# Optimization experiments

Measured on AMD Instinct MI355X. Metric: run time of the kernel, lower is better.

The kernel has to match this reference:

```python
import jax, jax.numpy as jnp
import numpy as np
import math

B, S, D, H = 4, 2048, 1024, 16
DK = D // H


def _rope_tables(seq_len, dim, dtype=jnp.float32):
    inv_freq = 1.0 / (10000.0 ** (jnp.arange(0, dim, 2, dtype=jnp.float32) / dim))
    t = jnp.arange(seq_len, dtype=jnp.float32)
    freqs = jnp.einsum('i,j->ij', t, inv_freq)          # [S, dim/2]
    emb = jnp.concatenate([freqs, freqs], axis=-1)       # [S, dim]
    return jnp.cos(emb).astype(dtype)[None, None], jnp.sin(emb).astype(dtype)[None, None]


def _apply_rope(x, cos, sin):
    # faithful to source: rotated = cat([-x[...,1::2], x[...,::2]], -1)
    x_rot = jnp.concatenate([-x[..., 1::2], x[..., ::2]], axis=-1)
    return x * cos + x_rot * sin


def setup_inputs() -> dict:
    key = jax.random.key(0)
    ks = jax.random.split(key, 12)
    scale = 1.0 / math.sqrt(D)
    inp = {
        'query': jax.random.normal(ks[0], (B, S, D), jnp.float32),
        'key':   jax.random.normal(ks[1], (B, S, D), jnp.float32),
        'value': jax.random.normal(ks[2], (B, S, D), jnp.float32),
        'mask':  jnp.tril(jnp.ones((S, S), jnp.int32))[None, None],  # causal [1,1,S,S]
        'w_q': jax.random.normal(ks[3], (D, D), jnp.float32) * scale,
        'b_q': jnp.zeros((D,), jnp.float32),
        'w_k': jax.random.normal(ks[4], (D, D), jnp.float32) * scale,
        'b_k': jnp.zeros((D,), jnp.float32),
        'w_v': jax.random.normal(ks[5], (D, D), jnp.float32) * scale,
        'b_v': jnp.zeros((D,), jnp.float32),
        'w_o': jax.random.normal(ks[6], (D, D), jnp.float32) * scale,
        'b_o': jnp.zeros((D,), jnp.float32),
    }
    return inp


def reference(query, key, value, mask, w_q, b_q, w_k, b_k, w_v, b_v, w_o, b_o):
    b, s, _ = query.shape
    # projections (torch Linear: x @ W.T + b), split heads -> [B,H,S,Dk]
    def proj(x, w, bias):
        return (x @ w.T + bias).reshape(b, -1, H, DK).transpose(0, 2, 1, 3)
    Q = proj(query, w_q, b_q)
    K = proj(key, w_k, b_k)
    V = proj(value, w_v, b_v)
    cos, sin = _rope_tables(s, DK, Q.dtype)
    Q = _apply_rope(Q, cos, sin)
    K = _apply_rope(K, cos, sin)
    scores = jnp.einsum('bhqd,bhkd->bhqk', Q, K) / math.sqrt(DK)
    scores = jnp.where(mask == 0, jnp.asarray(-1e9, scores.dtype), scores)
    attn = jax.nn.softmax(scores, axis=-1)
    ctx = jnp.einsum('bhqk,bhkd->bhqd', attn, V)
    ctx = ctx.transpose(0, 2, 1, 3).reshape(b, -1, D)
    return ctx @ w_o.T + b_o
```

## Files before the change

### kernel.cpp

```cpp
#include <hip/hip_runtime.h>
#include <hip/hip_bf16.h>
#include <math.h>

#define B_  4
#define S_  2048
#define D_  1024
#define H_  16
#define DK_ 64
#define M_  (B_ * S_)

typedef short short8 __attribute__((ext_vector_type(8)));
typedef float floatx4 __attribute__((ext_vector_type(4)));

__device__ inline unsigned short f2bf(float x) {
    unsigned u = __float_as_uint(x);
    u = (u + 0x7fff + ((u >> 16) & 1)) >> 16;
    return (unsigned short)u;
}
__device__ inline float bf2f(unsigned short h) {
    return __uint_as_float(((unsigned)h) << 16);
}

__device__ inline unsigned cvt_pk_bf16(float lo, float hi) {
    unsigned r;
    asm("v_cvt_pk_bf16_f32 %0, %1, %2" : "=v"(r) : "v"(lo), "v"(hi));
    return r;
}

template <int K>
__device__ inline float dpp_ror(float x) {
    return __uint_as_float((unsigned)__builtin_amdgcn_update_dpp(
        0, (int)__float_as_uint(x), 0x120 | K, 0xF, 0xF, true));
}
__device__ inline float rowmax16(float x) {
    x = fmaxf(x, dpp_ror<8>(x));
    x = fmaxf(x, dpp_ror<4>(x));
    x = fmaxf(x, dpp_ror<2>(x));
    x = fmaxf(x, dpp_ror<1>(x));
    return x;
}
__device__ inline float rowsum16(float x) {
    x += dpp_ror<8>(x);
    x += dpp_ror<4>(x);
    x += dpp_ror<2>(x);
    x += dpp_ror<1>(x);
    return x;
}

#define GLOAD_LDS16(g, l)                                          \
    __builtin_amdgcn_global_load_lds(                              \
        (const __attribute__((address_space(1))) void*)(g),        \
        (__attribute__((address_space(3))) void*)(l), 16, 0, 0)

__global__ __launch_bounds__(256) void cvt_inputs_kernel(
    const float* __restrict__ q, const float* __restrict__ k,
    const float* __restrict__ v, unsigned short* __restrict__ Ah)
{
    const int z = blockIdx.z;
    const float* src = (z == 0) ? q : (z == 1) ? k : v;
    unsigned short* dst = Ah + (size_t)z * M_ * D_;
    const size_t i = ((size_t)blockIdx.x * 256 + threadIdx.x) * 4;
    float4 f = *(const float4*)(src + i);
    ushort4 o;
    o.x = f2bf(f.x); o.y = f2bf(f.y); o.z = f2bf(f.z); o.w = f2bf(f.w);
    *(ushort4*)(dst + i) = o;
}

__global__ __launch_bounds__(256) void cvt_weights_kernel(
    const float* __restrict__ wq, const float* __restrict__ wk,
    const float* __restrict__ wv, const float* __restrict__ wo,
    unsigned short* __restrict__ Wh, unsigned short* __restrict__ Woh)
{
    const int z = blockIdx.z;
    const float* src = (z == 0) ? wq : (z == 1) ? wk : (z == 2) ? wv : wo;
    unsigned short* dst = (z < 3) ? (Wh + (size_t)z * D_ * D_) : Woh;
    const size_t i = ((size_t)blockIdx.x * 256 + threadIdx.x) * 4;
    float4 f = *(const float4*)(src + i);
    ushort4 o;
    o.x = f2bf(f.x); o.y = f2bf(f.y); o.z = f2bf(f.z); o.w = f2bf(f.w);
    *(ushort4*)(dst + i) = o;
}

template <int MODE>
__global__ __launch_bounds__(256) void gemm_bf16_kernel(
    const unsigned short* __restrict__ Ah, const unsigned short* __restrict__ Wh,
    const float* __restrict__ bq, const float* __restrict__ bk,
    const float* __restrict__ bv, void* __restrict__ outv)
{
    __shared__ __align__(16) unsigned short As[2][128 * 32];
    __shared__ __align__(16) unsigned short Bs[2][128 * 32];

    const int tid  = threadIdx.x;
    const int wave = tid >> 6;
    const int lane = tid & 63;
    const int quad = lane >> 4;
    const int l15  = lane & 15;
    const int z    = (MODE == 1) ? blockIdx.z : 0;
    const int m0   = blockIdx.x * 128;
    const int n0   = blockIdx.y * 128;
    const int wrow = (wave >> 1) * 64;
    const int wcol = (wave & 1) * 64;

    const unsigned short* A = Ah + (size_t)z * M_ * D_;
    const unsigned short* W = Wh + (size_t)z * D_ * D_;

    const int srow   = tid >> 2;
    const int schunk = (tid & 3) * 8;

#define STAGE_G(BUF, K0)                                                     \
    {                                                                        \
        GLOAD_LDS16(A + (size_t)(m0 + srow) * D_ + (K0) + schunk,            \
                    &As[BUF][wave * 512]);                                   \
        GLOAD_LDS16(W + (size_t)(n0 + srow) * D_ + (K0) + schunk,            \
                    &Bs[BUF][wave * 512]);                                   \
        GLOAD_LDS16(A + (size_t)(m0 + 64 + srow) * D_ + (K0) + schunk,       \
                    &As[BUF][2048 + wave * 512]);                            \
        GLOAD_LDS16(W + (size_t)(n0 + 64 + srow) * D_ + (K0) + schunk,       \
                    &Bs[BUF][2048 + wave * 512]);                            \
    }

    floatx4 acc[4][4] = {};

    STAGE_G(0, 0);
    __syncthreads();

    for (int k0 = 0; k0 < D_; k0 += 32) {
        const int cur = (k0 >> 5) & 1;
        if (k0 + 32 < D_) STAGE_G(cur ^ 1, k0 + 32);

        short8 af[4], bf[4];
#pragma unroll
        for (int i = 0; i < 4; ++i)
            af[i] = *(const short8*)&As[cur][(wrow + i * 16 + l15) * 32 + quad * 8];
#pragma unroll
        for (int j = 0; j < 4; ++j)
            bf[j] = *(const short8*)&Bs[cur][(wcol + j * 16 + l15) * 32 + quad * 8];
#pragma unroll
        for (int i = 0; i < 4; ++i)
#pragma unroll
            for (int j = 0; j < 4; ++j)
                acc[i][j] = __builtin_amdgcn_mfma_f32_16x16x32_bf16(
                    af[i], bf[j], acc[i][j], 0, 0, 0);

        __syncthreads();
    }
#undef STAGE_G

    const float* bias = (MODE == 0) ? bq : (z == 0) ? bq : (z == 1) ? bk : bv;

    if (MODE == 1) {
        unsigned short* Tw = (unsigned short*)As + wave * 16 * 68;
        const int bg = m0 >> 11;

        if (z == 2) {
            const int s0g = (m0 & (S_ - 1)) + wrow + quad * 16;
#pragma unroll
            for (int j = 0; j < 4; ++j) {
                const int n = n0 + wcol + j * 16 + l15;
                const float bn = bias[n];
#pragma unroll
                for (int i = 0; i < 4; ++i)
#pragma unroll
                    for (int reg = 0; reg < 4; ++reg)
                        Tw[l15 * 68 + i * 16 + quad * 4 + reg] =
                            f2bf(acc[i][j][reg] + bn);
                short8 r0 = *(const short8*)&Tw[l15 * 68 + quad * 16];
                short8 r1 = *(const short8*)&Tw[l15 * 68 + quad * 16 + 8];
                const int h = n >> 6, d = n & 63;
                unsigned short* dp = (unsigned short*)outv + 2 * (size_t)M_ * D_ +
                    (((size_t)(bg * H_ + h)) * DK_ + d) * S_ + s0g;
                *(short8*)(dp) = r0;
                *(short8*)(dp + 8) = r1;
            }
        } else {
            const int hq = (n0 + wcol) >> 6;
            const int sb = (m0 & (S_ - 1)) + wrow;
            unsigned short* dstz = (unsigned short*)outv + (size_t)z * M_ * D_;
#pragma unroll
            for (int i = 0; i < 4; ++i) {
#pragma unroll
                for (int j = 0; j < 4; ++j) {
                    const float bn = bias[n0 + wcol + j * 16 + l15];
#pragma unroll
                    for (int reg = 0; reg < 4; ++reg)
                        Tw[(quad * 4 + reg) * 68 + j * 16 + l15] =
                            f2bf(acc[i][j][reg] + bn);
                }
                short8 r0 = *(const short8*)&Tw[l15 * 68 + quad * 16];
                short8 r1 = *(const short8*)&Tw[l15 * 68 + quad * 16 + 8];
                unsigned short* dp = dstz +
                    (((size_t)bg * H_ + hq) * S_ + sb + i * 16 + l15) * DK_ +
                    quad * 16;
                *(short8*)dp = r0;
                *(short8*)(dp + 8) = r1;
            }
        }
        return;
    }

#pragma unroll
    for (int j = 0; j < 4; ++j) {
        const int n = n0 + wcol + j * 16 + l15;
        const float bn = bias[n];
#pragma unroll
        for (int i = 0; i < 4; ++i) {
#pragma unroll
            for (int reg = 0; reg < 4; ++reg) {
                const int m = m0 + wrow + i * 16 + quad * 4 + reg;
                ((float*)outv)[(size_t)m * D_ + n] = acc[i][j][reg] + bn;
            }
        }
    }
}

__global__ __launch_bounds__(256) void rope_kernel(unsigned short* __restrict__ Q,
                                                   unsigned short* __restrict__ K)
{
    const int wave = blockIdx.x * 4 + (threadIdx.x >> 6);
    const int lane = threadIdx.x & 63;
    const int rowsPer = B_ * H_ * S_;

    unsigned short* base = (wave < rowsPer) ? Q : K;
    const int row = (wave < rowsPer) ? wave : wave - rowsPer;
    const int s = row & (S_ - 1);

    unsigned short* p = base + (size_t)row * DK_;
    const float v = bf2f(p[lane]);

    const int j = lane & 31;
    const float inv_freq = 1.0f / powf(10000.0f, (float)(2 * j) / (float)DK_);
    const float ang = (float)s * inv_freq;
    const float c  = cosf(ang);
    const float si = sinf(ang);

    const int partner = (lane < 32) ? (2 * lane + 1) : (2 * (lane - 32));
    const float sign = (lane < 32) ? -1.0f : 1.0f;
    const float pv = __shfl(v, partner);

    p[lane] = f2bf(v * c + sign * pv * si);
}

#define KSTR 72

__global__ __launch_bounds__(256, 3) void attn_kernel(
    const unsigned short* __restrict__ Qh, const unsigned short* __restrict__ Kh,
    const unsigned short* __restrict__ Vt, unsigned short* __restrict__ ctx)
{
    __shared__ __align__(16) unsigned short Ks[2][64 * 64];
    __shared__ __align__(16) unsigned short Vs[2][64 * 64];
    __shared__ __align__(16) short Pw[4][16 * KSTR];

    const int tid  = threadIdx.x;
    const int wave = tid >> 6;
    const int lane = tid & 63;
    const int quad = lane >> 4;
    const int l15  = lane & 15;

    const int L  = blockIdx.x;
    const int bh = ((L >> 3) & 7) * 8 + (L & 7);
    const int qt = 31 - (L >> 6);
    const int q0 = qt * 64;

    const float c2 = 0.18033688011f;

    const unsigned short* Kbase = Kh + (size_t)bh * S_ * DK_;
    const unsigned short* Vbase = Vt + (size_t)bh * DK_ * S_;
    const int b = bh >> 4, h = bh & 15;

    short* Pme = &Pw[wave][0];

    const unsigned short* Qrow =
        Qh + ((size_t)bh * S_ + q0 + wave * 16 + l15) * DK_;
    short8 aQ[2];
    aQ[0] = *(const short8*)(Qrow + quad * 8);
    aQ[1] = *(const short8*)(Qrow + 32 + quad * 8);

    const int srow = lane >> 3;
    const int sg   = (lane & 7) ^ srow;
    const unsigned short* kSrc = Kbase + (size_t)(wave * 8 + srow) * DK_ + sg * 8;
    const unsigned short* vSrc = Vbase + (size_t)(wave * 8 + srow) * S_ + sg * 8;

    floatx4 acc[4] = {};
    float m_i[4] = {-INFINITY, -INFINITY, -INFINITY, -INFINITY};
    float l_i[4] = {0.f, 0.f, 0.f, 0.f};

#pragma unroll
    for (int rd = 0; rd < 2; ++rd) {
        GLOAD_LDS16(kSrc + (size_t)rd * 32 * DK_, &Ks[0][rd * 2048 + wave * 512]);
        GLOAD_LDS16(vSrc + (size_t)rd * 32 * S_,  &Vs[0][rd * 2048 + wave * 512]);
    }
    __syncthreads();

    int buf = 0;
    for (int j0 = 0; j0 <= q0; j0 += 64) {
        if (j0 + 64 <= q0) {
#pragma unroll
            for (int rd = 0; rd < 2; ++rd) {
                GLOAD_LDS16(kSrc + (size_t)(j0 + 64 + rd * 32) * DK_,
                            &Ks[buf ^ 1][rd * 2048 + wave * 512]);
                GLOAD_LDS16(vSrc + (j0 + 64) + (size_t)rd * 32 * S_,
                            &Vs[buf ^ 1][rd * 2048 + wave * 512]);
            }
        }

        floatx4 st[4] = {};
#pragma unroll
        for (int t = 0; t < 4; ++t)
#pragma unroll
            for (int kh = 0; kh < 2; ++kh) {
                short8 kf = *(const short8*)&Ks[buf][(t * 16 + l15) * 64 +
                              ((((kh << 2) + quad) ^ (l15 & 7)) << 3)];
                st[t] = __builtin_amdgcn_mfma_f32_16x16x32_bf16(
                    aQ[kh], kf, st[t], 0, 0, 0);
            }

        if (j0 == q0) {
#pragma unroll
            for (int t = 0; t < 4; ++t)
#pragma unroll
                for (int reg = 0; reg < 4; ++reg)
                    if (t * 16 + l15 > wave * 16 + quad * 4 + reg)
                        st[t][reg] = -INFINITY;
        }

#pragma unroll
        for (int reg = 0; reg < 4; ++reg) {
            float rmx = fmaxf(fmaxf(st[0][reg], st[1][reg]),
                              fmaxf(st[2][reg], st[3][reg]));
            rmx = rowmax16(rmx);
            const float pm = rmx * c2;
            if (__ballot(pm > m_i[reg] + 8.0f) != 0ull) {
                const float m2 = fmaxf(m_i[reg], pm);
                const float alpha = exp2f(m_i[reg] - m2);
                l_i[reg] *= alpha;
                m_i[reg] = m2;
                if (__ballot(alpha == 1.0f) != ~0ull) {
#pragma unroll
                    for (int t = 0; t < 4; ++t) acc[t][reg] *= alpha;
                }
            }
            const float m2v = m_i[reg];

            const float p0 = exp2f(fmaf(st[0][reg], c2, -m2v));
            const float p1 = exp2f(fmaf(st[1][reg], c2, -m2v));
            const float p2 = exp2f(fmaf(st[2][reg], c2, -m2v));
            const float p3 = exp2f(fmaf(st[3][reg], c2, -m2v));

            const unsigned pk01 = cvt_pk_bf16(p0, p1);
            const unsigned pk23 = cvt_pk_bf16(p2, p3);
            const int rbase = (quad * 4 + reg) * KSTR + l15;
            Pme[rbase]      = (short)(unsigned short)pk01;
            Pme[rbase + 16] = (short)(unsigned short)(pk01 >> 16);
            Pme[rbase + 32] = (short)(unsigned short)pk23;
            Pme[rbase + 48] = (short)(unsigned short)(pk23 >> 16);

            float rs = (p0 + p1) + (p2 + p3);
            rs = rowsum16(rs);
            l_i[reg] += rs;
        }

#pragma unroll
        for (int kh = 0; kh < 2; ++kh) {
            short8 aP = *(const short8*)&Pme[l15 * KSTR + kh * 32 + quad * 8];
#pragma unroll
            for (int t = 0; t < 4; ++t) {
                short8 vf = *(const short8*)&Vs[buf][(t * 16 + l15) * 64 +
                              ((((kh << 2) + quad) ^ (l15 & 7)) << 3)];
                acc[t] = __builtin_amdgcn_mfma_f32_16x16x32_bf16(
                    aP, vf, acc[t], 0, 0, 0);
            }
        }

        __syncthreads();
        buf ^= 1;
    }

#pragma unroll
    for (int reg = 0; reg < 4; ++reg) {
        const float inv = 1.0f / l_i[reg];
        const int q = q0 + wave * 16 + quad * 4 + reg;
        unsigned short* orow = ctx + ((size_t)b * S_ + q) * D_ + h * DK_;
#pragma unroll
        for (int t = 0; t < 4; ++t)
            orow[t * 16 + l15] = f2bf(acc[t][reg] * inv);
    }
}

extern "C" void kernel_launch(void* const* d_in, const int* in_sizes, int n_in,
                              void* d_out, int out_size, void* d_ws, size_t ws_size,
                              hipStream_t stream)
{
    const float* query = (const float*)d_in[0];
    const float* key   = (const float*)d_in[1];
    const float* value = (const float*)d_in[2];
    const float* w_q = (const float*)d_in[4];
    const float* b_q = (const float*)d_in[5];
    const float* w_k = (const float*)d_in[6];
    const float* b_k = (const float*)d_in[7];
    const float* w_v = (const float*)d_in[8];
    const float* b_v = (const float*)d_in[9];
    const float* w_o = (const float*)d_in[10];
    const float* b_o = (const float*)d_in[11];
    float* out = (float*)d_out;

    char* ws = (char*)d_ws;
    const size_t half = (size_t)M_ * D_ * sizeof(unsigned short);
    unsigned short* Ah   = (unsigned short*)(ws);
    unsigned short* Wh   = (unsigned short*)(ws + 3 * half);
    unsigned short* Woh  = (unsigned short*)(ws + 3 * half + 3 * half / 8);
    unsigned short* QKVb = (unsigned short*)(ws + 3 * half + 4 * half / 8);
    unsigned short* Ctxh = (unsigned short*)(ws + 6 * half + 4 * half / 8);

    cvt_inputs_kernel<<<dim3(M_ * D_ / 1024, 1, 3), 256, 0, stream>>>(
        query, key, value, Ah);
    cvt_weights_kernel<<<dim3(D_ * D_ / 1024, 1, 4), 256, 0, stream>>>(
        w_q, w_k, w_v, w_o, Wh, Woh);

    gemm_bf16_kernel<1><<<dim3(M_ / 128, D_ / 128, 3), 256, 0, stream>>>(
        Ah, Wh, b_q, b_k, b_v, QKVb);

    unsigned short* Qb = QKVb;
    unsigned short* Kb = QKVb + (size_t)M_ * D_;
    unsigned short* Vb = QKVb + 2 * (size_t)M_ * D_;

    rope_kernel<<<(2 * B_ * H_ * S_) / 4, 256, 0, stream>>>(Qb, Kb);

    attn_kernel<<<dim3(2048), 256, 0, stream>>>(Qb, Kb, Vb, Ctxh);

    gemm_bf16_kernel<0><<<dim3(M_ / 128, D_ / 128, 1), 256, 0, stream>>>(
        Ctxh, Woh, b_o, b_o, b_o, out);
}
```

Baseline: 447.1 us.

## Precompute RoPE cos/sin table, XOR-swizzle P tile, raise attention occupancy

Adds a small kernel that computes the per-position RoPE cos/sin table once, so the rope kernel reads a float2 instead of calling powf/cosf/sinf per element. In the attention kernel, the padded P scratch buffer (stride 72) is replaced by an unpadded 64-wide layout with an XOR swizzle to avoid LDS bank conflicts. That shrinks shared memory, and the launch-bounds occupancy hint goes from 3 to 4 blocks per CU. The table reuses the start of the workspace, which holds the already-consumed input copies. The higher occupancy hint may force register spilling.

Result: faster. 393.8 us (-11.9%).

```diff
diff --git a/kernel.cpp b/kernel.cpp
--- a/kernel.cpp
+++ b/kernel.cpp
@@ -213,8 +213,19 @@
     }
 }
 
+__global__ __launch_bounds__(256) void rope_tab_kernel(float* __restrict__ tab)
+{
+    const int idx = blockIdx.x * 256 + threadIdx.x;
+    const int s = idx >> 5, j = idx & 31;
+    const float inv_freq = exp2f((float)(2 * j) * (-13.28771237954945f / 64.f));
+    const float ang = (float)s * inv_freq;
+    tab[idx * 2]     = cosf(ang);
+    tab[idx * 2 + 1] = sinf(ang);
+}
+
 __global__ __launch_bounds__(256) void rope_kernel(unsigned short* __restrict__ Q,
-                                                   unsigned short* __restrict__ K)
+                                                   unsigned short* __restrict__ K,
+                                                   const float* __restrict__ tab)
 {
     const int wave = blockIdx.x * 4 + (threadIdx.x >> 6);
     const int lane = threadIdx.x & 63;
@@ -228,27 +239,22 @@
     const float v = bf2f(p[lane]);
 
     const int j = lane & 31;
-    const float inv_freq = 1.0f / powf(10000.0f, (float)(2 * j) / (float)DK_);
-    const float ang = (float)s * inv_freq;
-    const float c  = cosf(ang);
-    const float si = sinf(ang);
+    const float2 cs = ((const float2*)tab)[s * 32 + j];
 
     const int partner = (lane < 32) ? (2 * lane + 1) : (2 * (lane - 32));
     const float sign = (lane < 32) ? -1.0f : 1.0f;
     const float pv = __shfl(v, partner);
 
-    p[lane] = f2bf(v * c + sign * pv * si);
-}
-
-#define KSTR 72
-
-__global__ __launch_bounds__(256, 3) void attn_kernel(
+    p[lane] = f2bf(v * cs.x + sign * pv * cs.y);
+}
+
+__global__ __launch_bounds__(256, 4) void attn_kernel(
     const unsigned short* __restrict__ Qh, const unsigned short* __restrict__ Kh,
     const unsigned short* __restrict__ Vt, unsigned short* __restrict__ ctx)
 {
     __shared__ __align__(16) unsigned short Ks[2][64 * 64];
     __shared__ __align__(16) unsigned short Vs[2][64 * 64];
-    __shared__ __align__(16) short Pw[4][16 * KSTR];
+    __shared__ __align__(16) short Pw[4][16 * 64];
 
     const int tid  = threadIdx.x;
     const int wave = tid >> 6;
@@ -348,11 +354,14 @@
 
             const unsigned pk01 = cvt_pk_bf16(p0, p1);
             const unsigned pk23 = cvt_pk_bf16(p2, p3);
-            const int rbase = (quad * 4 + reg) * KSTR + l15;
-            Pme[rbase]      = (short)(unsigned short)pk01;
-            Pme[rbase + 16] = (short)(unsigned short)(pk01 >> 16);
-            Pme[rbase + 32] = (short)(unsigned short)pk23;
-            Pme[rbase + 48] = (short)(unsigned short)(pk23 >> 16);
+            const int r   = quad * 4 + reg;
+            const int sw  = r & 7;
+            const int ghi = l15 >> 3;
+            short* prow = Pme + r * 64 + (l15 & 7);
+            prow[((0 + ghi) ^ sw) << 3] = (short)(unsigned short)pk01;
+            prow[((2 + ghi) ^ sw) << 3] = (short)(unsigned short)(pk01 >> 16);
+            prow[((4 + ghi) ^ sw) << 3] = (short)(unsigned short)pk23;
+            prow[((6 + ghi) ^ sw) << 3] = (short)(unsigned short)(pk23 >> 16);
 
             float rs = (p0 + p1) + (p2 + p3);
             rs = rowsum16(rs);
@@ -361,7 +370,8 @@
 
 #pragma unroll
         for (int kh = 0; kh < 2; ++kh) {
-            short8 aP = *(const short8*)&Pme[l15 * KSTR + kh * 32 + quad * 8];
+            short8 aP = *(const short8*)&Pme[l15 * 64 +
+                          ((((kh << 2) + quad) ^ (l15 & 7)) << 3)];
 #pragma unroll
             for (int t = 0; t < 4; ++t) {
                 short8 vf = *(const short8*)&Vs[buf][(t * 16 + l15) * 64 +
@@ -410,6 +420,7 @@
     unsigned short* Woh  = (unsigned short*)(ws + 3 * half + 3 * half / 8);
     unsigned short* QKVb = (unsigned short*)(ws + 3 * half + 4 * half / 8);
     unsigned short* Ctxh = (unsigned short*)(ws + 6 * half + 4 * half / 8);
+    float*          Rtab = (float*)ws;
 
     cvt_inputs_kernel<<<dim3(M_ * D_ / 1024, 1, 3), 256, 0, stream>>>(
         query, key, value, Ah);
@@ -423,7 +434,8 @@
     unsigned short* Kb = QKVb + (size_t)M_ * D_;
     unsigned short* Vb = QKVb + 2 * (size_t)M_ * D_;
 
-    rope_kernel<<<(2 * B_ * H_ * S_) / 4, 256, 0, stream>>>(Qb, Kb);
+    rope_tab_kernel<<<(S_ * 32) / 256, 256, 0, stream>>>(Rtab);
+    rope_kernel<<<(2 * B_ * H_ * S_) / 4, 256, 0, stream>>>(Qb, Kb, Rtab);
 
     attn_kernel<<<dim3(2048), 256, 0, stream>>>(Qb, Kb, Vb, Ctxh);
 
```
